# Kernel tuning notes

Hardware: AMD Instinct MI355X
Metric: run time of the kernel (lower is better)

## Reference

```python
import jax, jax.numpy as jnp
import numpy as np

N_FREQ = 48  # tcnn Frequency encoding n_frequencies


def _freq_encode(x):
    # x: [N,3] in [0,1]; tcnn Frequency: sin/cos of x * 2^f * pi, f=0..F-1
    freqs = (2.0 ** jnp.arange(N_FREQ, dtype=jnp.float32)) * jnp.pi  # [F]
    ang = x[:, :, None] * freqs  # [N,3,F]
    enc = jnp.stack([jnp.sin(ang), jnp.cos(ang)], axis=-1)  # [N,3,F,2]
    return enc.reshape(x.shape[0], -1)  # [N, 3*F*2]


def _bilinear_sample(plane, coords):
    # plane: [R,R,F] (H,W,feat); coords: [N,2] in [-1,1], coords[:,0]->width(x), coords[:,1]->height(y)
    # matches torch grid_sample(align_corners=True, bilinear) for in-range coords
    R = plane.shape[0]
    gx = (coords[:, 0] + 1.0) * 0.5 * (R - 1)
    gy = (coords[:, 1] + 1.0) * 0.5 * (R - 1)
    x0f = jnp.clip(jnp.floor(gx), 0.0, R - 1)
    y0f = jnp.clip(jnp.floor(gy), 0.0, R - 1)
    x0 = x0f.astype(jnp.int32)
    y0 = y0f.astype(jnp.int32)
    x1 = jnp.minimum(x0 + 1, R - 1)
    y1 = jnp.minimum(y0 + 1, R - 1)
    wx = (gx - x0f)[:, None]
    wy = (gy - y0f)[:, None]
    v00 = plane[y0, x0]
    v01 = plane[y0, x1]
    v10 = plane[y1, x0]
    v11 = plane[y1, x1]
    return (v00 * (1 - wx) * (1 - wy) + v01 * wx * (1 - wy)
            + v10 * (1 - wx) * wy + v11 * wx * wy)  # [N,F]


def setup_inputs() -> dict:
    key = jax.random.key(0)
    ks = jax.random.split(key, 8)
    N = 524288
    res, fdim = 32, 16
    enc_dim = 3 * N_FREQ * 2  # 288
    d_in = enc_dim + fdim     # 304
    h = 64
    positions = jax.random.uniform(ks[0], (N, 3), dtype=jnp.float32)
    aabb = jnp.array([0.0, 0.0, 0.0, 1.0, 1.0, 1.0], dtype=jnp.float32)
    triplane = jax.random.normal(ks[1], (3, res, res, fdim), dtype=jnp.float32) * 0.001
    W0 = jax.random.normal(ks[2], (d_in, h), dtype=jnp.float32) / np.sqrt(d_in)
    W1 = jax.random.normal(ks[3], (h, h), dtype=jnp.float32) / np.sqrt(h)
    W2 = jax.random.normal(ks[4], (h, h), dtype=jnp.float32) / np.sqrt(h)
    W3 = jax.random.normal(ks[5], (h, 4), dtype=jnp.float32) / np.sqrt(h)
    return {"positions": positions, "aabb": aabb, "triplane": triplane,
            "W0": W0, "W1": W1, "W2": W2, "W3": W3}


def reference(positions, aabb, triplane, W0, W1, W2, W3):
    aabb_min, aabb_max = aabb[:3], aabb[3:]
    xn = (positions - aabb_min) / (aabb_max - aabb_min)          # normalized [0,1]
    sc = 2.0 * xn - 1.0                                          # scaled_coords in [-1,1]
    selector = jnp.all((xn > 0.0) & (xn < 1.0), axis=-1)
    # plane coordinate pairs as in the torch code
    coords = jnp.stack([
        jnp.stack([sc[:, 0], sc[:, 1]], axis=1),  # xy
        jnp.stack([sc[:, 0], sc[:, 2]], axis=1),  # xz
        jnp.stack([sc[:, 1], sc[:, 2]], axis=1),  # zy
    ], axis=0)  # [3,N,2]
    feats = jax.vmap(_bilinear_sample)(triplane, coords).sum(0)  # [N,fdim]
    h = jnp.concatenate([_freq_encode(xn), feats], axis=1)       # [N,304]
    h = jnp.sin(h @ W0)
    h = jnp.sin(h @ W1)
    h = jnp.sin(h @ W2)
    out = h @ W3                                                 # [N,4]
    rgb = jax.nn.sigmoid(out[:, :3])
    density = jnp.exp(out[:, 3:4] - 1.0) * selector[:, None]     # trunc_exp(x-1)
    return rgb, density
```

## Files before the change

### kernel.cpp

```cpp
#include <hip/hip_runtime.h>
#include <stdint.h>

typedef _Float16 half8  __attribute__((ext_vector_type(8)));
typedef _Float16 half2v __attribute__((ext_vector_type(2)));
typedef float f32x4 __attribute__((ext_vector_type(4)));

#define TPW 8
#define WPB 8
#define NT  512
#define W0S 304

__device__ __forceinline__ half2v pkrtz(float a, float b) {
    return __builtin_bit_cast(half2v, __builtin_amdgcn_cvt_pkrtz(a, b));
}

static __device__ __forceinline__ void mem_fence() {
    asm volatile("" ::: "memory");
}

__device__ __forceinline__ float bf2f(uint16_t u) {
    return __uint_as_float(((uint32_t)u) << 16);
}
__device__ __forceinline__ uint16_t f2bf(float f) {
    uint32_t u = __float_as_uint(f);
    u = (u + 0x7FFFu + ((u >> 16) & 1u)) >> 16;
    return (uint16_t)u;
}

template<bool BF>
__device__ __forceinline__ float lde(const void* p, uint32_t i) {
    if constexpr (BF) return bf2f(((const uint16_t*)p)[i]);
    else              return ((const float*)p)[i];
}
template<bool BF>
__device__ __forceinline__ void st1(void* p, uint32_t i, float v) {
    if constexpr (BF) ((uint16_t*)p)[i] = f2bf(v);
    else              ((float*)p)[i] = v;
}
template<bool BF>
__device__ __forceinline__ void ld8(const void* p, uint32_t i, float* o) {
    if constexpr (BF) {
        const uint4 c = *(const uint4*)((const uint16_t*)p + i);
        const uint32_t* pu = (const uint32_t*)&c;
#pragma unroll
        for (int j = 0; j < 4; ++j) {
            o[2 * j]     = __uint_as_float(pu[j] << 16);
            o[2 * j + 1] = __uint_as_float(pu[j] & 0xFFFF0000u);
        }
    } else {
        const float4 a = *(const float4*)((const float*)p + i);
        const float4 b = *(const float4*)((const float*)p + i + 4);
        o[0] = a.x; o[1] = a.y; o[2] = a.z; o[3] = a.w;
        o[4] = b.x; o[5] = b.y; o[6] = b.z; o[7] = b.w;
    }
}

__device__ __forceinline__ int hswz(int p, int g) {
    return p * 72 + ((g + 2 * (p >> 2)) & 7) * 8;
}

template<bool BF>
__device__ __forceinline__ void run_all(
    const void* __restrict__ posg, const void* __restrict__ aabbg,
    const void* __restrict__ tpg,
    const void* __restrict__ w0g, const void* __restrict__ w1g,
    const void* __restrict__ w2g, const void* __restrict__ w3g,
    void* __restrict__ outp, int npts,
    _Float16* w0t, _Float16* w1t, _Float16* w2t, _Float16* w3t, _Float16* hbuf)
{
    const int tid = threadIdx.x;
    const float I2PI = 0.15915494309189535f;

    for (int e = tid; e < 16; e += NT) w0t[64 * W0S + e] = (_Float16)0.0f;
    for (int e = tid; e < 304 * 64; e += NT) { int k = e >> 6, n = e & 63; w0t[n * W0S + k] = (_Float16)(lde<BF>(w0g, e) * I2PI); }
    for (int e = tid; e < 64 * 64;  e += NT) { int k = e >> 6, n = e & 63; w1t[n * 72 + k] = (_Float16)(lde<BF>(w1g, e) * I2PI);
                                               w2t[n * 72 + k] = (_Float16)(lde<BF>(w2g, e) * I2PI); }
    for (int e = tid; e < 64 * 4;   e += NT) { int k = e >> 2, n = e & 3;  w3t[n * 72 + k] = (_Float16)lde<BF>(w3g, e); }
    __syncthreads();

    const int w = tid >> 6, lane = tid & 63;
    const int m = lane & 15, q = lane >> 4;
    _Float16* hb = hbuf + w * (16 * 72);

    const float mn0 = lde<BF>(aabbg, 0), mn1 = lde<BF>(aabbg, 1), mn2 = lde<BF>(aabbg, 2);
    const float mx0 = lde<BF>(aabbg, 3), mx1 = lde<BF>(aabbg, 4), mx2 = lde<BF>(aabbg, 5);

    const double IH = 0x1.45f306dc9c883p-2;
    const double IL = -0x1.6b01ec5417056p-56;
    const float PIF  = 3.14159274101257324f;
    const f32x4 z4 = {0.f, 0.f, 0.f, 0.f};

    const int tile0 = (blockIdx.x * WPB + w) * TPW;

    auto xpose_sin = [&](const f32x4* a4) {
#pragma unroll
        for (int t4 = 0; t4 < 4; ++t4) {
            const int gw = 2 * t4 + (m >> 3);
#pragma unroll
            for (int rg = 0; rg < 4; ++rg)
                hb[hswz(4 * q + rg, gw) + (m & 7)] =
                    (_Float16)__builtin_amdgcn_sinf(a4[t4][rg]);
        }
    };
    auto hidden = [&](const _Float16* wt, f32x4* out) {
#pragma unroll
        for (int t4 = 0; t4 < 4; ++t4) out[t4] = z4;
#pragma unroll
        for (int c = 0; c < 2; ++c) {
            const half8 a = *(const half8*)&hb[hswz(m, 4 * c + q)];
#pragma unroll
            for (int t4 = 0; t4 < 4; ++t4) {
                const half8 b = *(const half8*)&wt[(t4 * 16 + m) * 72 + c * 32 + q * 8];
                out[t4] = __builtin_amdgcn_mfma_f32_16x16x32_f16(a, b, out[t4], 0, 0, 0);
            }
        }
    };

    float cp[2][3];
#pragma unroll
    for (int t = 0; t < 2; ++t) {
        const int pt = (tile0 + t) * 16 + m;
        cp[t][0] = lde<BF>(posg, 3 * pt + 0);
        cp[t][1] = lde<BF>(posg, 3 * pt + 1);
        cp[t][2] = lde<BF>(posg, 3 * pt + 2);
    }

    for (int io = 0; io < TPW / 2; ++io) {
        const int baseA = (tile0 + 2 * io) * 16;
        float pp[2][3];
#pragma unroll
        for (int t = 0; t < 2; ++t) {
            pp[t][0] = cp[t][0]; pp[t][1] = cp[t][1]; pp[t][2] = cp[t][2];
        }
        {
            const int nio = (io + 1 < TPW / 2) ? io + 1 : io;
#pragma unroll
            for (int t = 0; t < 2; ++t) {
                const int pt2 = (tile0 + 2 * nio + t) * 16 + m;
                cp[t][0] = lde<BF>(posg, 3 * pt2 + 0);
                cp[t][1] = lde<BF>(posg, 3 * pt2 + 1);
                cp[t][2] = lde<BF>(posg, 3 * pt2 + 2);
            }
        }

        bool sel[2];
        double wh[2][3], wl[2][3];
        float fe[2][8];
#pragma unroll
        for (int t = 0; t < 2; ++t) {
            float xn[3];
            xn[0] = (pp[t][0] - mn0) / (mx0 - mn0);
            xn[1] = (pp[t][1] - mn1) / (mx1 - mn1);
            xn[2] = (pp[t][2] - mn2) / (mx2 - mn2);
            sel[t] = xn[0] > 0.f && xn[0] < 1.f && xn[1] > 0.f && xn[1] < 1.f
                  && xn[2] > 0.f && xn[2] < 1.f;
#pragma unroll
            for (int d = 0; d < 3; ++d) {
                const float mf = xn[d] * PIF;
                const double md = (double)mf;
                const double hi = md * IH;
                const double r  = __builtin_fma(md, IH, -hi);
                wh[t][d] = hi;
                wl[t][d] = __builtin_fma(md, IL, r);
            }
#pragma unroll
            for (int j = 0; j < 8; ++j) fe[t][j] = 0.f;
            if (q < 2) {
                const int fo = q * 8;
                float g[3];
#pragma unroll
                for (int d = 0; d < 3; ++d) g[d] = xn[d] * 31.f;
                float v[8];
#pragma unroll
                for (int p = 0; p < 3; ++p) {
                    const float gx = (p == 2) ? g[1] : g[0];
                    const float gy = (p == 0) ? g[1] : g[2];
                    const float x0f = fminf(fmaxf(floorf(gx), 0.f), 31.f);
                    const float y0f = fminf(fmaxf(floorf(gy), 0.f), 31.f);
                    const int x0 = (int)x0f, y0 = (int)y0f;
                    int x1 = x0 + 1; if (x1 > 31) x1 = 31;
                    int y1 = y0 + 1; if (y1 > 31) y1 = 31;
                    const float wx = gx - x0f, wy = gy - y0f;
                    const float w00 = (1.f - wx) * (1.f - wy);
                    const float w01 = wx * (1.f - wy);
                    const float w10 = (1.f - wx) * wy;
                    const float w11 = wx * wy;
                    const uint32_t pb = p * 16384 + fo;
                    ld8<BF>(tpg, pb + y0 * 512 + x0 * 16, v);
#pragma unroll
                    for (int j = 0; j < 8; ++j) fe[t][j] += v[j] * w00;
                    ld8<BF>(tpg, pb + y0 * 512 + x1 * 16, v);
#pragma unroll
                    for (int j = 0; j < 8; ++j) fe[t][j] += v[j] * w01;
                    ld8<BF>(tpg, pb + y1 * 512 + x0 * 16, v);
#pragma unroll
                    for (int j = 0; j < 8; ++j) fe[t][j] += v[j] * w10;
                    ld8<BF>(tpg, pb + y1 * 512 + x1 * 16, v);
#pragma unroll
                    for (int j = 0; j < 8; ++j) fe[t][j] += v[j] * w11;
                }
            }
        }

        f32x4 acc0[2][4];
#pragma unroll
        for (int t = 0; t < 2; ++t)
#pragma unroll
            for (int t4 = 0; t4 < 4; ++t4) acc0[t][t4] = z4;

        {
            half8 au[2];
#pragma unroll
            for (int t = 0; t < 2; ++t) {
                union { half8 h8; half2v h2[4]; } u;
                if (q < 2) {
#pragma unroll
                    for (int i = 0; i < 4; ++i)
                        u.h2[i] = pkrtz(fe[t][2 * i], fe[t][2 * i + 1]);
                } else {
#pragma unroll
                    for (int j = 0; j < 8; ++j) u.h8[j] = (_Float16)0.f;
                }
                au[t] = u.h8;
            }
#pragma unroll
            for (int t4 = 0; t4 < 4; ++t4) {
                const half8 b = *(const half8*)&w0t[(t4 * 16 + m) * W0S + 288 + q * 8];
                acc0[0][t4] = __builtin_amdgcn_mfma_f32_16x16x32_f16(au[0], b, acc0[0][t4], 0, 0, 0);
                acc0[1][t4] = __builtin_amdgcn_mfma_f32_16x16x32_f16(au[1], b, acc0[1][t4], 0, 0, 0);
            }
        }
#pragma unroll
        for (int d = 0; d < 3; ++d) {
#pragma unroll
            for (int cc = 0; cc < 3; ++cc) {
                const int e0 = 16 * cc + 4 * q - 1;
                const double zp = __builtin_bit_cast(double, (uint64_t)(1023 + e0) << 52);
                half8 au[2];
#pragma unroll
                for (int t = 0; t < 2; ++t) {
                    const double z  = wh[t][d] * zp;
                    const double zl = wl[t][d] * zp;
                    const double fr = z - __builtin_floor(z);
                    const float tv = (float)(fr + zl);
                    float s = __builtin_amdgcn_sinf(tv);
                    float c = __builtin_amdgcn_cosf(tv);
                    union { half8 h8; half2v h2[4]; } u;
                    u.h2[0] = pkrtz(s, c);
#pragma unroll
                    for (int jj = 1; jj < 4; ++jj) {
                        const float t2 = s + s;
                        const float sn = t2 * c;
                        c = __builtin_fmaf(-t2, s, 1.0f);
                        s = sn;
                        u.h2[jj] = pkrtz(s, c);
                    }
                    au[t] = u.h8;
                }
                const int ch = 3 * d + cc;
#pragma unroll
                for (int t4 = 0; t4 < 4; ++t4) {
                    const half8 b = *(const half8*)&w0t[(t4 * 16 + m) * W0S + ch * 32 + q * 8];
                    acc0[0][t4] = __builtin_amdgcn_mfma_f32_16x16x32_f16(au[0], b, acc0[0][t4], 0, 0, 0);
                    acc0[1][t4] = __builtin_amdgcn_mfma_f32_16x16x32_f16(au[1], b, acc0[1][t4], 0, 0, 0);
                }
            }
        }

        f32x4 h1[2][4], h2[2][4];
#pragma unroll
        for (int t = 0; t < 2; ++t) {
            xpose_sin(acc0[t]);  mem_fence();
            hidden(w1t, h1[t]);  mem_fence();
        }
#pragma unroll
        for (int t = 0; t < 2; ++t) {
            xpose_sin(h1[t]);    mem_fence();
            hidden(w2t, h2[t]);  mem_fence();
        }
#pragma unroll
        for (int t = 0; t < 2; ++t) {
            xpose_sin(h2[t]);    mem_fence();
            f32x4 acc3 = z4;
#pragma unroll
            for (int c = 0; c < 2; ++c) {
                const half8 a = *(const half8*)&hb[hswz(m, 4 * c + q)];
                const half8 b = *(const half8*)&w3t[(m & 3) * 72 + c * 32 + q * 8];
                acc3 = __builtin_amdgcn_mfma_f32_16x16x32_f16(a, b, acc3, 0, 0, 0);
            }
            mem_fence();

            const int base = baseA + 16 * t;
            const unsigned long long bm = __ballot(sel[t]);
            if (m < 3) {
#pragma unroll
                for (int rg = 0; rg < 4; ++rg) {
                    const float s = 1.f / (1.f + __expf(-acc3[rg]));
                    st1<BF>(outp, (uint32_t)(base + 4 * q + rg) * 3u + m, s);
                }
            } else if (m == 3) {
                float dv[4];
#pragma unroll
                for (int rg = 0; rg < 4; ++rg) {
                    float dens = __expf(acc3[rg] - 1.f);
                    if (!((bm >> (4 * q + rg)) & 1ull)) dens = 0.f;
                    dv[rg] = dens;
                }
                const uint32_t di = 3u * (uint32_t)npts + (uint32_t)(base + 4 * q);
                if constexpr (BF) {
                    ushort4 pk;
                    pk.x = f2bf(dv[0]); pk.y = f2bf(dv[1]);
                    pk.z = f2bf(dv[2]); pk.w = f2bf(dv[3]);
                    *(ushort4*)((uint16_t*)outp + di) = pk;
                } else {
                    float4 pk = {dv[0], dv[1], dv[2], dv[3]};
                    *(float4*)((float*)outp + di) = pk;
                }
            }
        }
    }
}

__global__ __launch_bounds__(NT, 2)
void tri_mlp(const void* __restrict__ posg, const void* __restrict__ aabbg,
             const void* __restrict__ tpg,
             const void* __restrict__ w0g, const void* __restrict__ w1g,
             const void* __restrict__ w2g, const void* __restrict__ w3g,
             void* __restrict__ outp, int npts)
{
    __shared__ alignas(16) _Float16 w0t[64 * W0S + 16];
    __shared__ alignas(16) _Float16 w1t[64 * 72];
    __shared__ alignas(16) _Float16 w2t[64 * 72];
    __shared__ alignas(16) _Float16 w3t[4 * 72];
    __shared__ alignas(16) _Float16 hbuf[WPB * 16 * 72];

    const bool bf = (((const uint32_t*)aabbg)[2] != 0u);
    if (bf) run_all<true >(posg, aabbg, tpg, w0g, w1g, w2g, w3g, outp, npts, w0t, w1t, w2t, w3t, hbuf);
    else    run_all<false>(posg, aabbg, tpg, w0g, w1g, w2g, w3g, outp, npts, w0t, w1t, w2t, w3t, hbuf);
}

extern "C" void kernel_launch(void* const* d_in, const int* in_sizes, int n_in,
                              void* d_out, int out_size, void* d_ws, size_t ws_size,
                              hipStream_t stream) {
    const int npts = in_sizes[0] / 3;
    const int blocks = npts / (16 * WPB * TPW);
    tri_mlp<<<blocks, NT, 0, stream>>>(d_in[0], d_in[1], d_in[2], d_in[3],
                                       d_in[4], d_in[5], d_in[6], d_out, npts);
}
```

Baseline: 150.2 us.

## Pre-swizzle W0 into MFMA fragment layout in workspace; share triplane sampling across lanes

A small prep kernel converts W0 to fp16, scales it, and lays it out in MFMA B-fragment order in the workspace. The main kernel then reads W0 fragments straight from global/L2 instead of staging a ~39KB transposed copy in LDS, which shrinks LDS use and drops the per-block staging loop. Triplane sampling is also spread across all four lane quarters, one point-tile per half, and swapped back with ds_bpermute, so the previous q<2 lanes no longer do double work. The cost is a second launch and per-iteration global loads for W0 fragments that rely on cache hits.

```diff
diff --git a/kernel.cpp b/kernel.cpp
--- a/kernel.cpp
+++ b/kernel.cpp
@@ -8,7 +8,6 @@
 #define TPW 8
 #define WPB 8
 #define NT  512
-#define W0S 304
 
 __device__ __forceinline__ half2v pkrtz(float a, float b) {
     return __builtin_bit_cast(half2v, __builtin_amdgcn_cvt_pkrtz(a, b));
@@ -59,20 +58,38 @@
     return p * 72 + ((g + 2 * (p >> 2)) & 7) * 8;
 }
 
+__global__ void w0_prep(const void* __restrict__ w0g, const void* __restrict__ aabbg,
+                        uint16_t* __restrict__ ws)
+{
+    const bool bf = (((const uint32_t*)aabbg)[2] != 0u);
+    const float I2PI = 0.15915494309189535f;
+    for (int e = blockIdx.x * 256 + threadIdx.x; e < 20480; e += 8 * 256) {
+        const int j = e & 7, lane = (e >> 3) & 63, t4 = (e >> 9) & 3, ch = e >> 11;
+        const int m = lane & 15, q = lane >> 4;
+        const int k = ch * 32 + q * 8 + j, n = t4 * 16 + m;
+        float v = 0.f;
+        if (k < 304) {
+            v = (bf ? bf2f(((const uint16_t*)w0g)[k * 64 + n])
+                    : ((const float*)w0g)[k * 64 + n]) * I2PI;
+        }
+        const _Float16 h = (_Float16)v;
+        ws[e] = __builtin_bit_cast(uint16_t, h);
+    }
+}
+
 template<bool BF>
 __device__ __forceinline__ void run_all(
     const void* __restrict__ posg, const void* __restrict__ aabbg,
     const void* __restrict__ tpg,
-    const void* __restrict__ w0g, const void* __restrict__ w1g,
-    const void* __restrict__ w2g, const void* __restrict__ w3g,
+    const void* __restrict__ w1g, const void* __restrict__ w2g,
+    const void* __restrict__ w3g,
+    const half8* __restrict__ ws0,
     void* __restrict__ outp, int npts,
-    _Float16* w0t, _Float16* w1t, _Float16* w2t, _Float16* w3t, _Float16* hbuf)
+    _Float16* w1t, _Float16* w2t, _Float16* w3t, _Float16* hbuf)
 {
     const int tid = threadIdx.x;
     const float I2PI = 0.15915494309189535f;
 
-    for (int e = tid; e < 16; e += NT) w0t[64 * W0S + e] = (_Float16)0.0f;
-    for (int e = tid; e < 304 * 64; e += NT) { int k = e >> 6, n = e & 63; w0t[n * W0S + k] = (_Float16)(lde<BF>(w0g, e) * I2PI); }
     for (int e = tid; e < 64 * 64;  e += NT) { int k = e >> 6, n = e & 63; w1t[n * 72 + k] = (_Float16)(lde<BF>(w1g, e) * I2PI);
                                                w2t[n * 72 + k] = (_Float16)(lde<BF>(w2g, e) * I2PI); }
     for (int e = tid; e < 64 * 4;   e += NT) { int k = e >> 2, n = e & 3;  w3t[n * 72 + k] = (_Float16)lde<BF>(w3g, e); }
@@ -143,91 +160,95 @@
             }
         }
 
+        float xn[2][3];
         bool sel[2];
         double wh[2][3], wl[2][3];
-        float fe[2][8];
-#pragma unroll
-        for (int t = 0; t < 2; ++t) {
-            float xn[3];
-            xn[0] = (pp[t][0] - mn0) / (mx0 - mn0);
-            xn[1] = (pp[t][1] - mn1) / (mx1 - mn1);
-            xn[2] = (pp[t][2] - mn2) / (mx2 - mn2);
-            sel[t] = xn[0] > 0.f && xn[0] < 1.f && xn[1] > 0.f && xn[1] < 1.f
-                  && xn[2] > 0.f && xn[2] < 1.f;
+#pragma unroll
+        for (int t = 0; t < 2; ++t) {
+            xn[t][0] = (pp[t][0] - mn0) / (mx0 - mn0);
+            xn[t][1] = (pp[t][1] - mn1) / (mx1 - mn1);
+            xn[t][2] = (pp[t][2] - mn2) / (mx2 - mn2);
+            sel[t] = xn[t][0] > 0.f && xn[t][0] < 1.f && xn[t][1] > 0.f && xn[t][1] < 1.f
+                  && xn[t][2] > 0.f && xn[t][2] < 1.f;
 #pragma unroll
             for (int d = 0; d < 3; ++d) {
-                const float mf = xn[d] * PIF;
+                const float mf = xn[t][d] * PIF;
                 const double md = (double)mf;
                 const double hi = md * IH;
                 const double r  = __builtin_fma(md, IH, -hi);
                 wh[t][d] = hi;
                 wl[t][d] = __builtin_fma(md, IL, r);
             }
-#pragma unroll
-            for (int j = 0; j < 8; ++j) fe[t][j] = 0.f;
+        }
+
+        float fe[8];
+#pragma unroll
+        for (int j = 0; j < 8; ++j) fe[j] = 0.f;
+        {
+            const int tb = q >> 1, hf = q & 1;
+            const int fo = hf * 8;
+            float g[3];
+#pragma unroll
+            for (int d = 0; d < 3; ++d) g[d] = xn[tb][d] * 31.f;
+            float v[8];
+#pragma unroll
+            for (int p = 0; p < 3; ++p) {
+                const float gx = (p == 2) ? g[1] : g[0];
+                const float gy = (p == 0) ? g[1] : g[2];
+                const float x0f = fminf(fmaxf(floorf(gx), 0.f), 31.f);
+                const float y0f = fminf(fmaxf(floorf(gy), 0.f), 31.f);
+                const int x0 = (int)x0f, y0 = (int)y0f;
+                int x1 = x0 + 1; if (x1 > 31) x1 = 31;
+                int y1 = y0 + 1; if (y1 > 31) y1 = 31;
+                const float wx = gx - x0f, wy = gy - y0f;
+                const float w00 = (1.f - wx) * (1.f - wy);
+                const float w01 = wx * (1.f - wy);
+                const float w10 = (1.f - wx) * wy;
+                const float w11 = wx * wy;
+                const uint32_t pb = p * 16384 + fo;
+                ld8<BF>(tpg, pb + y0 * 512 + x0 * 16, v);
+#pragma unroll
+                for (int j = 0; j < 8; ++j) fe[j] += v[j] * w00;
+                ld8<BF>(tpg, pb + y0 * 512 + x1 * 16, v);
+#pragma unroll
+                for (int j = 0; j < 8; ++j) fe[j] += v[j] * w01;
+                ld8<BF>(tpg, pb + y1 * 512 + x0 * 16, v);
+#pragma unroll
+                for (int j = 0; j < 8; ++j) fe[j] += v[j] * w10;
+                ld8<BF>(tpg, pb + y1 * 512 + x1 * 16, v);
+#pragma unroll
+                for (int j = 0; j < 8; ++j) fe[j] += v[j] * w11;
+            }
+        }
+
+        f32x4 acc0[2][4];
+#pragma unroll
+        for (int t = 0; t < 2; ++t)
+#pragma unroll
+            for (int t4 = 0; t4 < 4; ++t4) acc0[t][t4] = z4;
+
+        {
+            uint32_t pk4[4], pl4[4];
+#pragma unroll
+            for (int i = 0; i < 4; ++i)
+                pk4[i] = __builtin_bit_cast(uint32_t, pkrtz(fe[2 * i], fe[2 * i + 1]));
+            const int badr = ((lane + 32) & 63) << 2;
+#pragma unroll
+            for (int i = 0; i < 4; ++i)
+                pl4[i] = (uint32_t)__builtin_amdgcn_ds_bpermute(badr, (int)pk4[i]);
+            union { uint32_t d[4]; half8 h8; } uA, uB;
             if (q < 2) {
-                const int fo = q * 8;
-                float g[3];
-#pragma unroll
-                for (int d = 0; d < 3; ++d) g[d] = xn[d] * 31.f;
-                float v[8];
-#pragma unroll
-                for (int p = 0; p < 3; ++p) {
-                    const float gx = (p == 2) ? g[1] : g[0];
-                    const float gy = (p == 0) ? g[1] : g[2];
-                    const float x0f = fminf(fmaxf(floorf(gx), 0.f), 31.f);
-                    const float y0f = fminf(fmaxf(floorf(gy), 0.f), 31.f);
-                    const int x0 = (int)x0f, y0 = (int)y0f;
-                    int x1 = x0 + 1; if (x1 > 31) x1 = 31;
-                    int y1 = y0 + 1; if (y1 > 31) y1 = 31;
-                    const float wx = gx - x0f, wy = gy - y0f;
-                    const float w00 = (1.f - wx) * (1.f - wy);
-                    const float w01 = wx * (1.f - wy);
-                    const float w10 = (1.f - wx) * wy;
-                    const float w11 = wx * wy;
-                    const uint32_t pb = p * 16384 + fo;
-                    ld8<BF>(tpg, pb + y0 * 512 + x0 * 16, v);
-#pragma unroll
-                    for (int j = 0; j < 8; ++j) fe[t][j] += v[j] * w00;
-                    ld8<BF>(tpg, pb + y0 * 512 + x1 * 16, v);
-#pragma unroll
-                    for (int j = 0; j < 8; ++j) fe[t][j] += v[j] * w01;
-                    ld8<BF>(tpg, pb + y1 * 512 + x0 * 16, v);
-#pragma unroll
-                    for (int j = 0; j < 8; ++j) fe[t][j] += v[j] * w10;
-                    ld8<BF>(tpg, pb + y1 * 512 + x1 * 16, v);
-#pragma unroll
-                    for (int j = 0; j < 8; ++j) fe[t][j] += v[j] * w11;
-                }
-            }
-        }
-
-        f32x4 acc0[2][4];
-#pragma unroll
-        for (int t = 0; t < 2; ++t)
-#pragma unroll
-            for (int t4 = 0; t4 < 4; ++t4) acc0[t][t4] = z4;
-
-        {
-            half8 au[2];
-#pragma unroll
-            for (int t = 0; t < 2; ++t) {
-                union { half8 h8; half2v h2[4]; } u;
-                if (q < 2) {
-#pragma unroll
-                    for (int i = 0; i < 4; ++i)
-                        u.h2[i] = pkrtz(fe[t][2 * i], fe[t][2 * i + 1]);
-                } else {
-#pragma unroll
-                    for (int j = 0; j < 8; ++j) u.h8[j] = (_Float16)0.f;
-                }
-                au[t] = u.h8;
+#pragma unroll
+                for (int i = 0; i < 4; ++i) { uA.d[i] = pk4[i]; uB.d[i] = pl4[i]; }
+            } else {
+#pragma unroll
+                for (int j = 0; j < 8; ++j) { uA.h8[j] = (_Float16)0.f; uB.h8[j] = (_Float16)0.f; }
             }
 #pragma unroll
             for (int t4 = 0; t4 < 4; ++t4) {
-                const half8 b = *(const half8*)&w0t[(t4 * 16 + m) * W0S + 288 + q * 8];
-                acc0[0][t4] = __builtin_amdgcn_mfma_f32_16x16x32_f16(au[0], b, acc0[0][t4], 0, 0, 0);
-                acc0[1][t4] = __builtin_amdgcn_mfma_f32_16x16x32_f16(au[1], b, acc0[1][t4], 0, 0, 0);
+                const half8 b = ws0[(9 * 4 + t4) * 64 + lane];
+                acc0[0][t4] = __builtin_amdgcn_mfma_f32_16x16x32_f16(uA.h8, b, acc0[0][t4], 0, 0, 0);
+                acc0[1][t4] = __builtin_amdgcn_mfma_f32_16x16x32_f16(uB.h8, b, acc0[1][t4], 0, 0, 0);
             }
         }
 #pragma unroll
@@ -260,7 +281,7 @@
                 const int ch = 3 * d + cc;
 #pragma unroll
                 for (int t4 = 0; t4 < 4; ++t4) {
-                    const half8 b = *(const half8*)&w0t[(t4 * 16 + m) * W0S + ch * 32 + q * 8];
+                    const half8 b = ws0[(ch * 4 + t4) * 64 + lane];
                     acc0[0][t4] = __builtin_amdgcn_mfma_f32_16x16x32_f16(au[0], b, acc0[0][t4], 0, 0, 0);
                     acc0[1][t4] = __builtin_amdgcn_mfma_f32_16x16x32_f16(au[1], b, acc0[1][t4], 0, 0, 0);
                 }
@@ -324,19 +345,19 @@
 __global__ __launch_bounds__(NT, 2)
 void tri_mlp(const void* __restrict__ posg, const void* __restrict__ aabbg,
              const void* __restrict__ tpg,
-             const void* __restrict__ w0g, const void* __restrict__ w1g,
-             const void* __restrict__ w2g, const void* __restrict__ w3g,
+             const void* __restrict__ w1g, const void* __restrict__ w2g,
+             const void* __restrict__ w3g,
+             const void* __restrict__ wsW0,
              void* __restrict__ outp, int npts)
 {
-    __shared__ alignas(16) _Float16 w0t[64 * W0S + 16];
     __shared__ alignas(16) _Float16 w1t[64 * 72];
     __shared__ alignas(16) _Float16 w2t[64 * 72];
     __shared__ alignas(16) _Float16 w3t[4 * 72];
     __shared__ alignas(16) _Float16 hbuf[WPB * 16 * 72];
 
     const bool bf = (((const uint32_t*)aabbg)[2] != 0u);
-    if (bf) run_all<true >(posg, aabbg, tpg, w0g, w1g, w2g, w3g, outp, npts, w0t, w1t, w2t, w3t, hbuf);
-    else    run_all<false>(posg, aabbg, tpg, w0g, w1g, w2g, w3g, outp, npts, w0t, w1t, w2t, w3t, hbuf);
+    if (bf) run_all<true >(posg, aabbg, tpg, w1g, w2g, w3g, (const half8*)wsW0, outp, npts, w1t, w2t, w3t, hbuf);
+    else    run_all<false>(posg, aabbg, tpg, w1g, w2g, w3g, (const half8*)wsW0, outp, npts, w1t, w2t, w3t, hbuf);
 }
 
 extern "C" void kernel_launch(void* const* d_in, const int* in_sizes, int n_in,
@@ -344,6 +365,7 @@
                               hipStream_t stream) {
     const int npts = in_sizes[0] / 3;
     const int blocks = npts / (16 * WPB * TPW);
-    tri_mlp<<<blocks, NT, 0, stream>>>(d_in[0], d_in[1], d_in[2], d_in[3],
-                                       d_in[4], d_in[5], d_in[6], d_out, npts);
-}
+    w0_prep<<<8, 256, 0, stream>>>(d_in[3], d_in[1], (uint16_t*)d_ws);
+    tri_mlp<<<blocks, NT, 0, stream>>>(d_in[0], d_in[1], d_in[2], d_in[4],
+                                       d_in[5], d_in[6], d_ws, d_out, npts);
+}
```

New measurement: 155.8 us. 1.04x slower.
